# Performance work log

Measured on AMD Instinct MI355X. Metric: run time of the kernel, lower is better.

Reference implementation:

```python
import jax, jax.numpy as jnp
import numpy as np

N_NODES = 100000
N_FEAT = 500
N_HID = 16
N_CLS = 7
N_EDGES = 3200000


def setup_inputs() -> dict:
    key = jax.random.key(0)
    k1, k2, k3, k4 = jax.random.split(key, 4)
    x = jax.random.normal(k1, (N_NODES, N_FEAT), dtype=jnp.float32)
    edge_index = jax.random.randint(k2, (2, N_EDGES), 0, N_NODES, dtype=jnp.int32)
    # Glorot-style init for the two GCNConv weight matrices
    W1 = jax.random.normal(k3, (N_FEAT, N_HID), dtype=jnp.float32) * (1.0 / np.sqrt(N_FEAT))
    b1 = jnp.zeros((N_HID,), dtype=jnp.float32)
    W2 = jax.random.normal(k4, (N_HID, N_CLS), dtype=jnp.float32) * (1.0 / np.sqrt(N_HID))
    b2 = jnp.zeros((N_CLS,), dtype=jnp.float32)
    return {"x": x, "edge_index": edge_index, "W1": W1, "b1": b1, "W2": W2, "b2": b2}


def _gcn_norm(edge_index, n_nodes):
    # Add self-loops, compute symmetric normalization D^-1/2 (A+I) D^-1/2
    loop = jnp.arange(n_nodes, dtype=edge_index.dtype)
    src = jnp.concatenate([edge_index[0], loop])  # [E+N]
    dst = jnp.concatenate([edge_index[1], loop])  # [E+N]
    deg = jax.ops.segment_sum(jnp.ones_like(dst, dtype=jnp.float32), dst, num_segments=n_nodes)
    dinv = jnp.where(deg > 0, jax.lax.rsqrt(deg), 0.0)
    norm = dinv[src] * dinv[dst]  # [E+N]
    return src, dst, norm


def _gcn_conv(h, W, b, src, dst, norm, n_nodes):
    m = h @ W                                   # [N, out] dense projection first (small out dim)
    agg = jax.ops.segment_sum(m[src] * norm[:, None], dst, num_segments=n_nodes)
    return agg + b


def reference(x, edge_index, W1, b1, W2, b2):
    n = x.shape[0]
    src, dst, norm = _gcn_norm(edge_index, n)
    h = jax.nn.relu(_gcn_conv(x, W1, b1, src, dst, norm, n))
    # dropout is identity in eval mode (training=False)
    logits = _gcn_conv(h, W2, b2, src, dst, norm, n)
    return jax.nn.log_softmax(logits, axis=1)
```

## Files before the change

kernel.cpp:

```cpp
#include <hip/hip_runtime.h>
#include <math.h>

#define N_NODES 100000
#define N_EDGES 3200000
#define N_FEAT  500
#define NF4     125
#define N_HID   16
#define N_CLS   7

#define BKT_SHIFT 7
#define BKT_SIZE  128
#define NBKT      782
#define NBLK_BIN  256
#define EDGES_PER_BLK 12500
#define COUNTS_LEN (NBKT * NBLK_BIN)
#define NBLK_SCANA (COUNTS_LEN / 256)
#define SBUF_CAP  5632

#define OFF_DINV   0
#define OFF_COUNTS 100000
#define OFF_BSUM   300192
#define OFF_ROWP   301216
#define OFF_BINNED 401220
#define OFF_SORTED 3601220
#define OFF_WP     6801220
#define OFF_M1S    6809412
#define OFF_M2S    7609412

typedef __attribute__((ext_vector_type(8))) short short8v;
typedef __attribute__((ext_vector_type(4))) float f32x4v;

__device__ inline unsigned short f2bf(float f) {
    unsigned int u = __float_as_uint(f);
    return (unsigned short)((u + 0x7FFF + ((u >> 16) & 1)) >> 16);
}
__device__ inline float bf2f(unsigned short h) {
    return __uint_as_float((unsigned int)h << 16);
}

__device__ inline void gload16(const void* g, void* l) {
    __builtin_amdgcn_global_load_lds(
        (const __attribute__((address_space(1))) void*)g,
        (__attribute__((address_space(3))) void*)l, 16, 0, 0);
}

__global__ void hist(const int* __restrict__ dst, int* __restrict__ counts) {
    __shared__ int cnt[NBKT];
    int t = threadIdx.x, b = blockIdx.x;
    for (int i = t; i < NBKT; i += 256) cnt[i] = 0;
    __syncthreads();
    int e0 = b * EDGES_PER_BLK;
    for (int e = e0 + t; e < e0 + EDGES_PER_BLK; e += 256)
        atomicAdd(&cnt[dst[e] >> BKT_SHIFT], 1);
    __syncthreads();
    for (int i = t; i < NBKT; i += 256)
        counts[i * NBLK_BIN + b] = cnt[i];
}

__global__ void scanA(int* __restrict__ counts, int* __restrict__ bsum) {
    __shared__ int s[256];
    int t = threadIdx.x;
    int i = blockIdx.x * 256 + t;
    int v = counts[i];
    s[t] = v;
    __syncthreads();
    for (int off = 1; off < 256; off <<= 1) {
        int a = (t >= off) ? s[t - off] : 0;
        __syncthreads();
        s[t] += a;
        __syncthreads();
    }
    counts[i] = s[t] - v;
    if (t == 255) bsum[blockIdx.x] = s[255];
}

__global__ void scanB(int* __restrict__ bsum) {
    __shared__ int s[1024];
    int t = threadIdx.x;
    int v = (t < NBLK_SCANA) ? bsum[t] : 0;
    s[t] = v;
    __syncthreads();
    for (int off = 1; off < 1024; off <<= 1) {
        int a = (t >= off) ? s[t - off] : 0;
        __syncthreads();
        s[t] += a;
        __syncthreads();
    }
    if (t < NBLK_SCANA) bsum[t] = s[t] - v;
}

__global__ void binpass(const int* __restrict__ src, const int* __restrict__ dst,
                        const int* __restrict__ counts, const int* __restrict__ bsum,
                        unsigned int* __restrict__ binned) {
    __shared__ int cur[NBKT];
    int t = threadIdx.x, b = blockIdx.x;
    for (int i = t; i < NBKT; i += 256) cur[i] = counts[i * NBLK_BIN + b] + bsum[i];
    __syncthreads();
    int e0 = b * EDGES_PER_BLK;
    for (int e = e0 + t; e < e0 + EDGES_PER_BLK; e += 256) {
        int d = dst[e];
        int pos = atomicAdd(&cur[d >> BKT_SHIFT], 1);
        binned[pos] = (unsigned int)src[e] | ((unsigned int)(d & (BKT_SIZE - 1)) << 17);
    }
}

__global__ __launch_bounds__(512) void sortA(const unsigned int* __restrict__ binned,
        const int* __restrict__ counts, const int* __restrict__ bsum,
        int* __restrict__ rowptr, float* __restrict__ dinv) {
    __shared__ int cnt[BKT_SIZE];
    __shared__ int sc[BKT_SIZE];
    int t = threadIdx.x, b = blockIdx.x;
    int beg = counts[b * NBLK_BIN] + bsum[b];
    int end = (b < NBKT - 1) ? counts[(b + 1) * NBLK_BIN] + bsum[b + 1] : N_EDGES;
    if (t < BKT_SIZE) cnt[t] = 0;
    __syncthreads();
    for (int e = beg + t; e < end; e += 512)
        atomicAdd(&cnt[(binned[e] >> 17) & (BKT_SIZE - 1)], 1);
    __syncthreads();
    int v = (t < BKT_SIZE) ? cnt[t] : 0;
    if (t < BKT_SIZE) sc[t] = v;
    __syncthreads();
    for (int off = 1; off < BKT_SIZE; off <<= 1) {
        int a = (t < BKT_SIZE && t >= off) ? sc[t - off] : 0;
        __syncthreads();
        if (t < BKT_SIZE) sc[t] += a;
        __syncthreads();
    }
    if (t < BKT_SIZE) {
        int g = b * BKT_SIZE + t;
        if (g < N_NODES) {
            rowptr[g] = beg + sc[t] - v;
            dinv[g] = rsqrtf((float)v + 1.0f);
        }
    }
    if (b == 0 && t == 0) rowptr[N_NODES] = N_EDGES;
}

__global__ void wpack(const float* __restrict__ W1, uint4* __restrict__ wp) {
    int p = blockIdx.x * 256 + threadIdx.x;
    if (p >= 1024) return;
    int s = p >> 6, l = p & 63;
    int col = l & 15, kb = s * 32 + (l >> 4) * 8;
    unsigned int hw[4], lw[4];
#pragma unroll
    for (int d = 0; d < 4; ++d) {
        unsigned int hpair = 0, lpair = 0;
#pragma unroll
        for (int e = 0; e < 2; ++e) {
            int k = kb + d * 2 + e;
            float w0 = (k < N_FEAT) ? W1[k * 16 + col] : 0.f;
            unsigned int u = __float_as_uint(w0);
            unsigned int uh = u & 0xFFFF0000u;
            float res = w0 - __uint_as_float(uh);
            hpair |= (uh >> 16) << (16 * e);
            lpair |= (unsigned int)f2bf(res) << (16 * e);
        }
        hw[d] = hpair; lw[d] = lpair;
    }
    wp[p] = make_uint4(hw[0], hw[1], hw[2], hw[3]);
    wp[1024 + p] = make_uint4(lw[0], lw[1], lw[2], lw[3]);
}

#define G1_NBLK 1563

__device__ inline void split8(const float4 a, const float4 b, short8v& hi, short8v& lo) {
    float f[8] = {a.x, a.y, a.z, a.w, b.x, b.y, b.z, b.w};
#pragma unroll
    for (int i = 0; i < 8; ++i) {
        unsigned int u = __float_as_uint(f[i]);
        unsigned int uh = u & 0xFFFF0000u;
        hi[i] = (short)(u >> 16);
        lo[i] = (short)f2bf(f[i] - __uint_as_float(uh));
    }
}

__global__ __launch_bounds__(256) void gemm1(const float* __restrict__ x,
        const uint4* __restrict__ wp, const float* __restrict__ dinv,
        unsigned short* __restrict__ m1s) {
    __shared__ float lds[2][2048];
    const int t = threadIdx.x, b = blockIdx.x;
    const int lane = t & 63, w = t >> 6;
    const int rowbase = b * 64;
    const char* xb = (const char*)x;

    size_t gbase[2], gtail[2];
#pragma unroll
    for (int j = 0; j < 2; ++j) {
        int i = j * 256 + t;
        int row = i >> 3;
        int u = i & 7;
        int inner = (u * 16) ^ ((row & 7) << 4);
        int grow = rowbase + row; if (grow >= N_NODES) grow = 0;
        gbase[j] = (size_t)grow * 2000 + (size_t)inner;
        int tf = 480 + (inner >> 2);
        gtail[j] = (tf < 500) ? gbase[j] + 1920 : (size_t)0;
    }

    const int r16 = lane & 15, g = lane >> 4;
    const int lrow = w * 16 + r16;
    const int sw = (lrow & 7) << 4;
    const int off1 = lrow * 128 + ((g * 32) ^ sw);
    const int off2 = lrow * 128 + ((g * 32 + 16) ^ sw);

    f32x4v acc = {0.f, 0.f, 0.f, 0.f};

    gload16(xb + gbase[0], (void*)&lds[0][w * 256]);
    gload16(xb + gbase[1], (void*)&lds[0][1024 + w * 256]);
    __syncthreads();

    int cur = 0;
    for (int s = 0; s < 16; ++s) {
        if (s < 15) {
            int sn = s + 1;
            size_t a0 = (sn < 15) ? gbase[0] + (size_t)sn * 128 : gtail[0];
            size_t a1 = (sn < 15) ? gbase[1] + (size_t)sn * 128 : gtail[1];
            gload16(xb + a0, (void*)&lds[cur ^ 1][w * 256]);
            gload16(xb + a1, (void*)&lds[cur ^ 1][1024 + w * 256]);
        }
        short8v bh = *reinterpret_cast<const short8v*>(&wp[s * 64 + lane]);
        short8v bl = *reinterpret_cast<const short8v*>(&wp[1024 + s * 64 + lane]);
        const char* lb = (const char*)&lds[cur][0];
        float4 fa = *(const float4*)(lb + off1);
        float4 fb = *(const float4*)(lb + off2);
        short8v ah, al;
        split8(fa, fb, ah, al);
        acc = __builtin_amdgcn_mfma_f32_16x16x32_bf16(ah, bh, acc, 0, 0, 0);
        acc = __builtin_amdgcn_mfma_f32_16x16x32_bf16(al, bh, acc, 0, 0, 0);
        acc = __builtin_amdgcn_mfma_f32_16x16x32_bf16(ah, bl, acc, 0, 0, 0);
        __syncthreads();
        cur ^= 1;
    }

#pragma unroll
    for (int j = 0; j < 4; ++j) {
        int r = rowbase + w * 16 + g * 4 + j;
        if (r < N_NODES) m1s[(size_t)r * 16 + r16] = f2bf(acc[j] * dinv[r]);
    }
}

__global__ __launch_bounds__(512) void sortAgg1(const unsigned int* __restrict__ binned,
        const int* __restrict__ counts, const int* __restrict__ bsum,
        const int* __restrict__ rowptr, const float* __restrict__ dinv,
        const unsigned short* __restrict__ m1s, const float* __restrict__ b1,
        const float* __restrict__ W2, unsigned int* __restrict__ sorted,
        unsigned short* __restrict__ m2s) {
    __shared__ unsigned int sbuf[SBUF_CAP];
    __shared__ int cur[BKT_SIZE];
    __shared__ float acc[BKT_SIZE * 17];
    __shared__ float sW2[N_HID * N_CLS];
    __shared__ float sb1[N_HID];
    int t = threadIdx.x, b = blockIdx.x;
    if (t < N_HID * N_CLS) sW2[t] = W2[t];
    if (t < N_HID) sb1[t] = b1[t];
    int beg = counts[b * NBLK_BIN] + bsum[b];
    int end = (b < NBKT - 1) ? counts[(b + 1) * NBLK_BIN] + bsum[b + 1] : N_EDGES;
    if (t < BKT_SIZE) {
        int g = b * BKT_SIZE + t;
        cur[t] = ((g < N_NODES) ? rowptr[g] : end) - beg;
    }
    __syncthreads();
    for (int e = beg + t; e < end; e += 512) {
        unsigned int u = binned[e];
        int pos = atomicAdd(&cur[(u >> 17) & (BKT_SIZE - 1)], 1);
        if (pos < SBUF_CAP) sbuf[pos] = u & 0x1FFFF;
    }
    __syncthreads();
    int n = end - beg;
    for (int i = t; i < n; i += 512) sorted[beg + i] = sbuf[i];
    {
        int nn = t >> 2, q = t & 3;
        int g = b * BKT_SIZE + nn;
        float a0 = 0.f, a1 = 0.f, a2 = 0.f, a3 = 0.f;
        if (g < N_NODES) {
            int lbeg = rowptr[g] - beg;
            int lend = ((g + 1 <= N_NODES) ? rowptr[g + 1] : N_EDGES) - beg;
            int p = lbeg;
            for (; p + 1 < lend; p += 2) {
                unsigned int s0 = sbuf[p], s1 = sbuf[p + 1];
                uint2 w0 = *(const uint2*)&m1s[(size_t)s0 * 16 + q * 4];
                uint2 w1 = *(const uint2*)&m1s[(size_t)s1 * 16 + q * 4];
                a0 += __uint_as_float(w0.x << 16);
                a1 += __uint_as_float(w0.x & 0xFFFF0000u);
                a2 += __uint_as_float(w0.y << 16);
                a3 += __uint_as_float(w0.y & 0xFFFF0000u);
                a0 += __uint_as_float(w1.x << 16);
                a1 += __uint_as_float(w1.x & 0xFFFF0000u);
                a2 += __uint_as_float(w1.y << 16);
                a3 += __uint_as_float(w1.y & 0xFFFF0000u);
            }
            if (p < lend) {
                unsigned int s0 = sbuf[p];
                uint2 w0 = *(const uint2*)&m1s[(size_t)s0 * 16 + q * 4];
                a0 += __uint_as_float(w0.x << 16);
                a1 += __uint_as_float(w0.x & 0xFFFF0000u);
                a2 += __uint_as_float(w0.y << 16);
                a3 += __uint_as_float(w0.y & 0xFFFF0000u);
            }
        }
        __syncthreads();
        float* ap = &acc[nn * 17 + q * 4];
        ap[0] = a0; ap[1] = a1; ap[2] = a2; ap[3] = a3;
    }
    __syncthreads();
    for (int idx = t; idx < BKT_SIZE * 16; idx += 512) {
        int nn = idx >> 4, jj = idx & 15;
        int gg = b * BKT_SIZE + nn;
        if (gg < N_NODES) {
            float di = dinv[gg];
            float hv = di * (acc[nn * 17 + jj] + bf2f(m1s[(size_t)gg * 16 + jj])) + sb1[jj];
            acc[nn * 17 + jj] = hv > 0.f ? hv : 0.f;
        }
    }
    __syncthreads();
    for (int idx = t; idx < BKT_SIZE * 8; idx += 512) {
        int nn = idx >> 3, cc = idx & 7;
        int gg = b * BKT_SIZE + nn;
        if (gg < N_NODES) {
            float sum = 0.f;
            if (cc < N_CLS) {
#pragma unroll
                for (int jj = 0; jj < N_HID; ++jj) sum += acc[nn * 17 + jj] * sW2[jj * 7 + cc];
                sum *= dinv[gg];
            }
            m2s[(size_t)gg * 8 + cc] = f2bf(sum);
        }
    }
}

__global__ __launch_bounds__(256) void agg2(const unsigned int* __restrict__ sorted,
        const int* __restrict__ rowptr, const float* __restrict__ dinv,
        const unsigned short* __restrict__ m2s, const float* __restrict__ b2,
        float* __restrict__ out) {
    __shared__ float acc[BKT_SIZE * 9];
    int t = threadIdx.x, b = blockIdx.x;
    int n = t >> 1, q = t & 1;
    int g = b * BKT_SIZE + n;
    float a0 = 0.f, a1 = 0.f, a2 = 0.f, a3 = 0.f;
    if (g < N_NODES) {
        int beg = rowptr[g], end = rowptr[g + 1];
        int p = beg;
        for (; p + 1 < end; p += 2) {
            unsigned int s0 = sorted[p], s1 = sorted[p + 1];
            uint2 w0 = *(const uint2*)&m2s[(size_t)s0 * 8 + q * 4];
            uint2 w1 = *(const uint2*)&m2s[(size_t)s1 * 8 + q * 4];
            a0 += __uint_as_float(w0.x << 16);
            a1 += __uint_as_float(w0.x & 0xFFFF0000u);
            a2 += __uint_as_float(w0.y << 16);
            a3 += __uint_as_float(w0.y & 0xFFFF0000u);
            a0 += __uint_as_float(w1.x << 16);
            a1 += __uint_as_float(w1.x & 0xFFFF0000u);
            a2 += __uint_as_float(w1.y << 16);
            a3 += __uint_as_float(w1.y & 0xFFFF0000u);
        }
        if (p < end) {
            unsigned int s0 = sorted[p];
            uint2 w0 = *(const uint2*)&m2s[(size_t)s0 * 8 + q * 4];
            a0 += __uint_as_float(w0.x << 16);
            a1 += __uint_as_float(w0.x & 0xFFFF0000u);
            a2 += __uint_as_float(w0.y << 16);
            a3 += __uint_as_float(w0.y & 0xFFFF0000u);
        }
    }
    float* ap = &acc[n * 9 + q * 4];
    ap[0] = a0; ap[1] = a1; ap[2] = a2; ap[3] = a3;
    __syncthreads();
    int j = t & 7;
    for (int pass = 0; pass < 4; ++pass) {
        int nn = (t >> 3) + pass * 32;
        int gg = b * BKT_SIZE + nn;
        bool valid = (gg < N_NODES) && (j < N_CLS);
        float v = -1e30f;
        if (valid) {
            float di = dinv[gg];
            v = di * (acc[nn * 9 + j] + bf2f(m2s[(size_t)gg * 8 + j])) + b2[j];
        }
        float mx = v;
#pragma unroll
        for (int off = 1; off < 8; off <<= 1) mx = fmaxf(mx, __shfl_xor(mx, off, 8));
        float ex = valid ? expf(v - mx) : 0.f;
        float sum = ex;
#pragma unroll
        for (int off = 1; off < 8; off <<= 1) sum += __shfl_xor(sum, off, 8);
        float ls = mx + logf(sum);
        if (valid) out[(size_t)gg * 7 + j] = v - ls;
    }
}

extern "C" void kernel_launch(void* const* d_in, const int* in_sizes, int n_in,
                              void* d_out, int out_size, void* d_ws, size_t ws_size,
                              hipStream_t stream) {
    const float* x  = (const float*)d_in[0];
    const int*   ei = (const int*)d_in[1];
    const float* W1 = (const float*)d_in[2];
    const float* b1 = (const float*)d_in[3];
    const float* W2 = (const float*)d_in[4];
    const float* b2 = (const float*)d_in[5];
    float* out = (float*)d_out;
    char*  wsb = (char*)d_ws;

    const int* src = ei;
    const int* dst = ei + N_EDGES;

    float*          dinv   = (float*)wsb + OFF_DINV;
    int*            counts = (int*)wsb + OFF_COUNTS;
    int*            bsum   = (int*)wsb + OFF_BSUM;
    int*            rowptr = (int*)wsb + OFF_ROWP;
    unsigned int*   binned = (unsigned int*)wsb + OFF_BINNED;
    unsigned int*   sorted = (unsigned int*)wsb + OFF_SORTED;
    uint4*          wp     = (uint4*)((int*)wsb + OFF_WP);
    unsigned short* m1s    = (unsigned short*)(wsb + (size_t)OFF_M1S * 4);
    unsigned short* m2s    = (unsigned short*)(wsb + (size_t)OFF_M2S * 4);

    hist     <<<NBLK_BIN, 256, 0, stream>>>(dst, counts);
    scanA    <<<NBLK_SCANA, 256, 0, stream>>>(counts, bsum);
    scanB    <<<1, 1024, 0, stream>>>(bsum);
    binpass  <<<NBLK_BIN, 256, 0, stream>>>(src, dst, counts, bsum, binned);
    sortA    <<<NBKT, 512, 0, stream>>>(binned, counts, bsum, rowptr, dinv);
    wpack    <<<4, 256, 0, stream>>>(W1, wp);
    gemm1    <<<G1_NBLK, 256, 0, stream>>>(x, wp, dinv, m1s);
    sortAgg1 <<<NBKT, 512, 0, stream>>>(binned, counts, bsum, rowptr, dinv,
                                        m1s, b1, W2, sorted, m2s);
    agg2     <<<NBKT, 256, 0, stream>>>(sorted, rowptr, dinv, m2s, b2, out);
}
```

Baseline: 477.4 us.

## Load GEMM1 inputs directly into registers and vectorize edge binning loads

```diff
diff --git a/kernel.cpp b/kernel.cpp
--- a/kernel.cpp
+++ b/kernel.cpp
@@ -38,20 +38,19 @@
     return __uint_as_float((unsigned int)h << 16);
 }
 
-__device__ inline void gload16(const void* g, void* l) {
-    __builtin_amdgcn_global_load_lds(
-        (const __attribute__((address_space(1))) void*)g,
-        (__attribute__((address_space(3))) void*)l, 16, 0, 0);
-}
-
 __global__ void hist(const int* __restrict__ dst, int* __restrict__ counts) {
     __shared__ int cnt[NBKT];
     int t = threadIdx.x, b = blockIdx.x;
     for (int i = t; i < NBKT; i += 256) cnt[i] = 0;
     __syncthreads();
-    int e0 = b * EDGES_PER_BLK;
-    for (int e = e0 + t; e < e0 + EDGES_PER_BLK; e += 256)
-        atomicAdd(&cnt[dst[e] >> BKT_SHIFT], 1);
+    const int4* d4 = (const int4*)(dst + b * EDGES_PER_BLK);
+    for (int k = t; k < EDGES_PER_BLK / 4; k += 256) {
+        int4 d = d4[k];
+        atomicAdd(&cnt[d.x >> BKT_SHIFT], 1);
+        atomicAdd(&cnt[d.y >> BKT_SHIFT], 1);
+        atomicAdd(&cnt[d.z >> BKT_SHIFT], 1);
+        atomicAdd(&cnt[d.w >> BKT_SHIFT], 1);
+    }
     __syncthreads();
     for (int i = t; i < NBKT; i += 256)
         counts[i * NBLK_BIN + b] = cnt[i];
@@ -96,11 +95,20 @@
     int t = threadIdx.x, b = blockIdx.x;
     for (int i = t; i < NBKT; i += 256) cur[i] = counts[i * NBLK_BIN + b] + bsum[i];
     __syncthreads();
-    int e0 = b * EDGES_PER_BLK;
-    for (int e = e0 + t; e < e0 + EDGES_PER_BLK; e += 256) {
-        int d = dst[e];
-        int pos = atomicAdd(&cur[d >> BKT_SHIFT], 1);
-        binned[pos] = (unsigned int)src[e] | ((unsigned int)(d & (BKT_SIZE - 1)) << 17);
+    const int4* s4 = (const int4*)(src + b * EDGES_PER_BLK);
+    const int4* d4 = (const int4*)(dst + b * EDGES_PER_BLK);
+    for (int k = t; k < EDGES_PER_BLK / 4; k += 256) {
+        int4 d = d4[k];
+        int4 s = s4[k];
+        int pos;
+        pos = atomicAdd(&cur[d.x >> BKT_SHIFT], 1);
+        binned[pos] = (unsigned int)s.x | ((unsigned int)(d.x & (BKT_SIZE - 1)) << 17);
+        pos = atomicAdd(&cur[d.y >> BKT_SHIFT], 1);
+        binned[pos] = (unsigned int)s.y | ((unsigned int)(d.y & (BKT_SIZE - 1)) << 17);
+        pos = atomicAdd(&cur[d.z >> BKT_SHIFT], 1);
+        binned[pos] = (unsigned int)s.z | ((unsigned int)(d.z & (BKT_SIZE - 1)) << 17);
+        pos = atomicAdd(&cur[d.w >> BKT_SHIFT], 1);
+        binned[pos] = (unsigned int)s.w | ((unsigned int)(d.w & (BKT_SIZE - 1)) << 17);
     }
 }
 
@@ -177,63 +185,53 @@
 __global__ __launch_bounds__(256) void gemm1(const float* __restrict__ x,
         const uint4* __restrict__ wp, const float* __restrict__ dinv,
         unsigned short* __restrict__ m1s) {
-    __shared__ float lds[2][2048];
+    __shared__ uint4 swp[2048];
     const int t = threadIdx.x, b = blockIdx.x;
     const int lane = t & 63, w = t >> 6;
-    const int rowbase = b * 64;
-    const char* xb = (const char*)x;
-
-    size_t gbase[2], gtail[2];
-#pragma unroll
-    for (int j = 0; j < 2; ++j) {
-        int i = j * 256 + t;
-        int row = i >> 3;
-        int u = i & 7;
-        int inner = (u * 16) ^ ((row & 7) << 4);
-        int grow = rowbase + row; if (grow >= N_NODES) grow = 0;
-        gbase[j] = (size_t)grow * 2000 + (size_t)inner;
-        int tf = 480 + (inner >> 2);
-        gtail[j] = (tf < 500) ? gbase[j] + 1920 : (size_t)0;
-    }
+#pragma unroll
+    for (int i = 0; i < 8; ++i) swp[i * 256 + t] = wp[i * 256 + t];
+    __syncthreads();
 
     const int r16 = lane & 15, g = lane >> 4;
-    const int lrow = w * 16 + r16;
-    const int sw = (lrow & 7) << 4;
-    const int off1 = lrow * 128 + ((g * 32) ^ sw);
-    const int off2 = lrow * 128 + ((g * 32 + 16) ^ sw);
+    const int rowbase = b * 64 + w * 16;
+    const int row = rowbase + r16;
+    const int srow = (row < N_NODES) ? row : 0;
+    const float* pA = x + (size_t)srow * N_FEAT + g * 8;
+    const float* t0 = (g <= 2) ? pA + 480 : x;
+    const float* t1 = (g <= 1) ? pA + 484 : x;
+
+    float4 a0_0 = *(const float4*)(pA);       float4 a1_0 = *(const float4*)(pA + 4);
+    float4 a0_1 = *(const float4*)(pA + 32);  float4 a1_1 = *(const float4*)(pA + 36);
+    float4 a0_2 = *(const float4*)(pA + 64);  float4 a1_2 = *(const float4*)(pA + 68);
 
     f32x4v acc = {0.f, 0.f, 0.f, 0.f};
-
-    gload16(xb + gbase[0], (void*)&lds[0][w * 256]);
-    gload16(xb + gbase[1], (void*)&lds[0][1024 + w * 256]);
-    __syncthreads();
-
-    int cur = 0;
+#pragma unroll
     for (int s = 0; s < 16; ++s) {
-        if (s < 15) {
-            int sn = s + 1;
-            size_t a0 = (sn < 15) ? gbase[0] + (size_t)sn * 128 : gtail[0];
-            size_t a1 = (sn < 15) ? gbase[1] + (size_t)sn * 128 : gtail[1];
-            gload16(xb + a0, (void*)&lds[cur ^ 1][w * 256]);
-            gload16(xb + a1, (void*)&lds[cur ^ 1][1024 + w * 256]);
-        }
-        short8v bh = *reinterpret_cast<const short8v*>(&wp[s * 64 + lane]);
-        short8v bl = *reinterpret_cast<const short8v*>(&wp[1024 + s * 64 + lane]);
-        const char* lb = (const char*)&lds[cur][0];
-        float4 fa = *(const float4*)(lb + off1);
-        float4 fb = *(const float4*)(lb + off2);
+        float4 xa, xb;
+        if ((s % 3) == 0)      { xa = a0_0; xb = a1_0; }
+        else if ((s % 3) == 1) { xa = a0_1; xb = a1_1; }
+        else                   { xa = a0_2; xb = a1_2; }
         short8v ah, al;
-        split8(fa, fb, ah, al);
+        split8(xa, xb, ah, al);
+        if (s < 13) {
+            const float* p = (s == 12) ? t0 : pA + (s + 3) * 32;
+            const float* q = (s == 12) ? t1 : pA + (s + 3) * 32 + 4;
+            float4 n0 = *(const float4*)p;
+            float4 n1 = *(const float4*)q;
+            if ((s % 3) == 0)      { a0_0 = n0; a1_0 = n1; }
+            else if ((s % 3) == 1) { a0_1 = n0; a1_1 = n1; }
+            else                   { a0_2 = n0; a1_2 = n1; }
+        }
+        short8v bh = *reinterpret_cast<const short8v*>(&swp[s * 64 + lane]);
+        short8v bl = *reinterpret_cast<const short8v*>(&swp[1024 + s * 64 + lane]);
         acc = __builtin_amdgcn_mfma_f32_16x16x32_bf16(ah, bh, acc, 0, 0, 0);
         acc = __builtin_amdgcn_mfma_f32_16x16x32_bf16(al, bh, acc, 0, 0, 0);
         acc = __builtin_amdgcn_mfma_f32_16x16x32_bf16(ah, bl, acc, 0, 0, 0);
-        __syncthreads();
-        cur ^= 1;
     }
 
 #pragma unroll
     for (int j = 0; j < 4; ++j) {
-        int r = rowbase + w * 16 + g * 4 + j;
+        int r = rowbase + g * 4 + j;
         if (r < N_NODES) m1s[(size_t)r * 16 + r16] = f2bf(acc[j] * dinv[r]);
     }
 }
```

After: 438.1 us. 1.09x faster.
